# Performance work log

Hardware: AMD Instinct MI355X
Metric: run time of the kernel (lower is better)

## Reference

```python
import jax, jax.numpy as jnp
import numpy as np

N_NODES = 50000
N_EDGES = 800000
F_NODE = 128
F_TASK = 128
HID = 64
HEADS = 4
BATCH = 16
NEG_SLOPE = 0.2


def setup_inputs() -> dict:
    key = jax.random.key(0)
    ks = jax.random.split(key, 20)
    rn = lambda k, sh, s=0.05: jax.random.normal(k, sh, dtype=jnp.float32) * s
    return {
        "x": rn(ks[0], (N_NODES, F_NODE), 1.0),
        "edge_index": jax.random.randint(ks[1], (2, N_EDGES), 0, N_NODES, dtype=jnp.int32),
        "task_feat": rn(ks[2], (BATCH, F_TASK), 1.0),
        # GAT layer 1 (F_NODE -> HEADS*HID, concat)
        "W1": rn(ks[3], (F_NODE, HEADS * HID)),
        "att_src1": rn(ks[4], (HEADS, HID)),
        "att_dst1": rn(ks[5], (HEADS, HID)),
        "b1": jnp.zeros((HEADS * HID,), jnp.float32),
        # GAT layer 2 (HEADS*HID -> HID, 1 head, mean/no-concat)
        "W2": rn(ks[6], (HEADS * HID, HID)),
        "att_src2": rn(ks[7], (1, HID)),
        "att_dst2": rn(ks[8], (1, HID)),
        "b2": jnp.zeros((HID,), jnp.float32),
        # task encoder MLP
        "te_W1": rn(ks[9], (F_TASK, HID)),
        "te_b1": jnp.zeros((HID,), jnp.float32),
        "te_W2": rn(ks[10], (HID, HID)),
        "te_b2": jnp.zeros((HID,), jnp.float32),
        # classifier MLP (2*HID -> HID -> 1)
        "cl_W1": rn(ks[11], (2 * HID, HID)),
        "cl_b1": jnp.zeros((HID,), jnp.float32),
        "cl_W2": rn(ks[12], (HID, 1)),
        "cl_b2": jnp.zeros((1,), jnp.float32),
    }


def _gat(x, src, dst, W, a_src, a_dst, bias, concat):
    """PyG-style GATConv: self-loops, per-dst segment softmax, scatter-add."""
    n = x.shape[0]
    heads, ch = a_src.shape
    h = (x @ W).reshape(n, heads, ch)                       # [N,H,C]
    alpha_s = jnp.einsum("nhc,hc->nh", h, a_src)            # [N,H]
    alpha_d = jnp.einsum("nhc,hc->nh", h, a_dst)
    loop = jnp.arange(n, dtype=src.dtype)                   # add self-loops
    s = jnp.concatenate([src, loop])
    d = jnp.concatenate([dst, loop])
    e = jax.nn.leaky_relu(alpha_s[s] + alpha_d[d], NEG_SLOPE)   # [E+N,H]
    m = jax.lax.stop_gradient(jax.ops.segment_max(e, d, num_segments=n))
    ex = jnp.exp(e - m[d])
    den = jax.ops.segment_sum(ex, d, num_segments=n)
    alpha = ex / (den[d] + 1e-16)                           # [E+N,H]
    out = jax.ops.segment_sum(h[s] * alpha[:, :, None], d, num_segments=n)
    out = out.reshape(n, heads * ch) if concat else out.mean(axis=1)
    return out + bias


def reference(x, edge_index, task_feat, W1, att_src1, att_dst1, b1,
              W2, att_src2, att_dst2, b2, te_W1, te_b1, te_W2, te_b2,
              cl_W1, cl_b1, cl_W2, cl_b2):
    src, dst = edge_index[0], edge_index[1]
    h = jax.nn.elu(_gat(x, src, dst, W1, att_src1, att_dst1, b1, True))
    h = jax.nn.elu(_gat(h, src, dst, W2, att_src2, att_dst2, b2, False))  # [N,HID]
    t = jax.nn.relu(task_feat @ te_W1 + te_b1) @ te_W2 + te_b2            # [B,HID]
    # classifier on concat([h_exp, t_exp]) == split first linear into two halves
    Wh, Wt = cl_W1[:HID], cl_W1[HID:]
    z = jax.nn.relu((h @ Wh)[None, :, :] + (t @ Wt)[:, None, :] + cl_b1)  # [B,N,HID]
    scores = (z @ cl_W2)[..., 0] + cl_b2[0]                               # [B,N]
    return scores
```

## Files before the change

### kernel.cpp

```cpp
#include <hip/hip_runtime.h>
#include <hip/hip_fp16.h>

#define NN 50000
#define NE 800000
#define FN 128
#define HH 256
#define HID 64
#define NBKT 196
#define CHUNK 4000
#define REGCAP 8192

typedef _Float16 f16x8 __attribute__((ext_vector_type(8)));
typedef float f32x4 __attribute__((ext_vector_type(4)));

__device__ __forceinline__ float lrelu(float v){ return v >= 0.f ? v : 0.2f * v; }
__device__ __forceinline__ float elu_(float v){ return v > 0.f ? v : expm1f(v); }

__device__ __forceinline__ void unp4(const float2 r, float& f0, float& f1, float& f2, float& f3){
  const __half2* hp = (const __half2*)&r;
  float2 a = __half22float2(hp[0]);
  float2 b = __half22float2(hp[1]);
  f0 = a.x; f1 = a.y; f2 = b.x; f3 = b.y;
}

__global__ void k_misc(const float* __restrict__ W2, const float* __restrict__ W1,
                       __half* __restrict__ Bp, __half* __restrict__ Bp1, __half* __restrict__ Bwh,
                       const float* __restrict__ task, const float* __restrict__ W1t,
                       const float* __restrict__ b1t, const float* __restrict__ W2t,
                       const float* __restrict__ b2t, const float* __restrict__ clW1,
                       const float* __restrict__ clb1, float* __restrict__ tWb,
                       int* __restrict__ binCnt){
  int bid = blockIdx.x, t = threadIdx.x;
  if (bid < 26){
    int f = bid * 256 + t;
    if (f < 2048){
      int lane = f & 63;
      int ct = (f >> 6) & 3, kt = f >> 8;
      int kbase = kt * 32 + (lane >> 4) * 8;
      int col = ct * 16 + (lane & 15);
#pragma unroll
      for (int i = 0; i < 8; ++i)
        Bp[(size_t)f * 8 + i] = (__half)W2[(kbase + i) * HID + col];
    } else if (f < 6144){
      int g = f - 2048;
      int lane = g & 63;
      int ct = (g >> 6) & 15, kt = g >> 10;
      int kbase = kt * 32 + (lane >> 4) * 8;
      int col = ct * 16 + (lane & 15);
#pragma unroll
      for (int i = 0; i < 8; ++i)
        Bp1[(size_t)g * 8 + i] = (__half)W1[(kbase + i) * HH + col];
    } else {
      int g = f - 6144;
      int lane = g & 63;
      int ct = (g >> 6) & 3, kt = g >> 8;
      int kbase = kt * 32 + (lane >> 4) * 8;
      int col = ct * 16 + (lane & 15);
#pragma unroll
      for (int i = 0; i < 8; ++i)
        Bwh[(size_t)g * 8 + i] = (__half)clW1[(kbase + i) * HID + col];
    }
  } else {
    binCnt[t] = 0;
    __shared__ float t1[16][64];
    __shared__ float t2[16][64];
    for (int idx = t; idx < 1024; idx += 256){
      int b = idx >> 6, c = idx & 63;
      float acc = b1t[c];
      for (int k = 0; k < 128; ++k) acc = fmaf(task[b*128 + k], W1t[k*64 + c], acc);
      t1[b][c] = fmaxf(acc, 0.f);
    }
    __syncthreads();
    for (int idx = t; idx < 1024; idx += 256){
      int b = idx >> 6, c = idx & 63;
      float acc = b2t[c];
      for (int k = 0; k < 64; ++k) acc = fmaf(t1[b][k], W2t[k*64 + c], acc);
      t2[b][c] = acc;
    }
    __syncthreads();
    for (int idx = t; idx < 1024; idx += 256){
      int b = idx >> 6, c = idx & 63;
      float acc = clb1[c];
      for (int k = 0; k < 64; ++k) acc = fmaf(t2[b][k], clW1[(64 + k)*64 + c], acc);
      tWb[idx] = acc;
    }
  }
}

__global__ void k_binGemm(const int* __restrict__ ei, int* __restrict__ binCnt,
                          unsigned* __restrict__ pr,
                          const float* __restrict__ x, const __half* __restrict__ Bp1,
                          const float* __restrict__ as1, const float* __restrict__ ad1,
                          __half* __restrict__ h1h, float* __restrict__ als, float* __restrict__ ald){
  __shared__ int hist[NBKT];
  __shared__ int lstart[NBKT];
  __shared__ int gpos[NBKT];
  __shared__ int cnt[NBKT];
  __shared__ unsigned stage[CHUNK];
  int bid = blockIdx.x, t = threadIdx.x;
  if (bid < 200){
    int e_base = bid * CHUNK;
    if (t < NBKT){ hist[t] = 0; cnt[t] = 0; }
    __syncthreads();
    for (int i = t; i < CHUNK; i += 256)
      atomicAdd(&hist[ei[NE + e_base + i] >> 8], 1);
    __syncthreads();
    {
      int lane = t & 63, wvi = t >> 6;
      int v = (t < NBKT) ? hist[t] : 0;
      int iv = v;
#pragma unroll
      for (int off = 1; off < 64; off <<= 1){
        int u = __shfl_up(iv, off);
        if (lane >= off) iv += u;
      }
      __shared__ int wsum[4];
      if (lane == 63) wsum[wvi] = iv;
      __syncthreads();
      int add = 0;
      for (int w = 0; w < wvi; ++w) add += wsum[w];
      iv += add;
      if (t < NBKT){
        lstart[t] = iv - v;
        gpos[t] = (v > 0) ? atomicAdd(&binCnt[t], v) : 0;
      }
    }
    __syncthreads();
    for (int i = t; i < CHUNK; i += 256){
      int e = e_base + i;
      int s = ei[e], d = ei[NE + e];
      int bb = d >> 8;
      int r = atomicAdd(&cnt[bb], 1);
      stage[lstart[bb] + r] = (unsigned)s | ((unsigned)(d & 255) << 16) | ((unsigned)bb << 24);
    }
    __syncthreads();
    for (int i = t; i < CHUNK; i += 256){
      unsigned p = stage[i];
      int bb = p >> 24;
      pr[(size_t)bb * REGCAP + gpos[bb] + (i - lstart[bb])] = p;
    }
    return;
  }
  int blk = bid - 200;
  int wv = t >> 6, lane = t & 63;
  int n0 = blk * 64 + wv * 16;
  int arow = n0 + (lane & 15);
  if (arow > NN - 1) arow = NN - 1;
  const float* xbase = x + (size_t)arow * FN + (lane >> 4) * 8;
  const f16x8* bbase = (const f16x8*)Bp1 + lane;

  f32x4 acc[16];
#pragma unroll
  for (int ct = 0; ct < 16; ++ct) acc[ct] = (f32x4){0.f,0.f,0.f,0.f};

#pragma unroll
  for (int kt = 0; kt < 4; ++kt){
    float4 xa = *(const float4*)(xbase + kt * 32);
    float4 xb = *(const float4*)(xbase + kt * 32 + 4);
    f16x8 a;
    a[0] = (_Float16)xa.x; a[1] = (_Float16)xa.y; a[2] = (_Float16)xa.z; a[3] = (_Float16)xa.w;
    a[4] = (_Float16)xb.x; a[5] = (_Float16)xb.y; a[6] = (_Float16)xb.z; a[7] = (_Float16)xb.w;
#pragma unroll
    for (int ct = 0; ct < 16; ++ct)
      acc[ct] = __builtin_amdgcn_mfma_f32_16x16x32_f16(a, bbase[(kt*16 + ct) * 64], acc[ct], 0, 0, 0);
  }

  int c4 = lane & 15, g4 = lane >> 4;
#pragma unroll
  for (int ct = 0; ct < 16; ++ct){
#pragma unroll
    for (int i = 0; i < 4; ++i){
      int n = n0 + g4 * 4 + i;
      if (n < NN) h1h[(size_t)n * HH + ct * 16 + c4] = (__half)acc[ct][i];
    }
  }
#pragma unroll
  for (int h = 0; h < 4; ++h){
    float sa0 = as1[(h*4+0)*16 + c4], sa1 = as1[(h*4+1)*16 + c4];
    float sa2 = as1[(h*4+2)*16 + c4], sa3 = as1[(h*4+3)*16 + c4];
    float da0 = ad1[(h*4+0)*16 + c4], da1 = ad1[(h*4+1)*16 + c4];
    float da2 = ad1[(h*4+2)*16 + c4], da3 = ad1[(h*4+3)*16 + c4];
#pragma unroll
    for (int i = 0; i < 4; ++i){
      float vs = acc[h*4+0][i]*sa0 + acc[h*4+1][i]*sa1 + acc[h*4+2][i]*sa2 + acc[h*4+3][i]*sa3;
      float vd = acc[h*4+0][i]*da0 + acc[h*4+1][i]*da1 + acc[h*4+2][i]*da2 + acc[h*4+3][i]*da3;
#pragma unroll
      for (int off = 1; off < 16; off <<= 1){
        vs += __shfl_xor(vs, off);
        vd += __shfl_xor(vd, off);
      }
      if (c4 == 0){
        int n = n0 + g4 * 4 + i;
        if (n < NN){ als[n*4 + h] = vs; ald[n*4 + h] = vd; }
      }
    }
  }
}

__global__ void k_rsplace(const int* __restrict__ binCnt, const unsigned* __restrict__ pr,
                          int* __restrict__ rs, int* __restrict__ csr){
  __shared__ int bbase[256];
  __shared__ int hist[256];
  __shared__ int lp[256];
  __shared__ int wsA[4];
  __shared__ int wsB[4];
  int b = blockIdx.x, t = threadIdx.x;
  int lane = t & 63, wv = t >> 6;
  {
    int v = (t < NBKT) ? binCnt[t] : 0;
    int iv = v;
#pragma unroll
    for (int off = 1; off < 64; off <<= 1){
      int u = __shfl_up(iv, off);
      if (lane >= off) iv += u;
    }
    if (lane == 63) wsA[wv] = iv;
    __syncthreads();
    int add = 0;
    for (int w = 0; w < wv; ++w) add += wsA[w];
    bbase[t] = iv + add - v;
    hist[t] = 0;
  }
  __syncthreads();
  int myBase = bbase[b];
  int myCnt  = binCnt[b];
  const unsigned* reg = pr + (size_t)b * REGCAP;
  for (int i = t; i < myCnt; i += 256)
    atomicAdd(&hist[(reg[i] >> 16) & 255], 1);
  __syncthreads();
  int excl;
  {
    int v = hist[t];
    int iv = v;
#pragma unroll
    for (int off = 1; off < 64; off <<= 1){
      int u = __shfl_up(iv, off);
      if (lane >= off) iv += u;
    }
    if (lane == 63) wsB[wv] = iv;
    __syncthreads();
    int add = 0;
    for (int w = 0; w < wv; ++w) add += wsB[w];
    excl = myBase + iv + add - v;
    lp[t] = excl;
  }
  int idx = b * 256 + t;
  if (idx < NN) rs[idx] = excl;
  if (b == 0 && t == 0) rs[NN] = NE;
  __syncthreads();
  for (int i = t; i < myCnt; i += 256){
    unsigned p = reg[i];
    int pos = atomicAdd(&lp[(p >> 16) & 255], 1);
    csr[pos] = (int)(p & 0xFFFFu);
  }
}

__global__ void k_agg1m(const int* __restrict__ rs, const int* __restrict__ csr,
                        const __half* __restrict__ h1h, const float* __restrict__ als,
                        const float* __restrict__ ald, const float* __restrict__ b1,
                        __half* __restrict__ g1h){
  int t = threadIdx.x, wv = t >> 6, lane = t & 63;
  int head = lane >> 4, q = lane & 15;
  int n = blockIdx.x * 4 + wv;
  int e0 = rs[n], e1 = rs[n + 1];
  int deg = e1 - e0;
  float adh = ald[n*4 + head];

  float w0r = 0.f, w1r = 0.f, w2r = 0.f, w3r = 0.f;
  int   s0r = 0,   s1r = 0,   s2r = 0,   s3r = 0;
  float den = 0.f;
  if (q      < deg){ s0r = csr[e0 + q];      w0r = expf(lrelu(als[s0r*4+head] + adh)); den += w0r; }
  if (q + 16 < deg){ s1r = csr[e0 + 16 + q]; w1r = expf(lrelu(als[s1r*4+head] + adh)); den += w1r; }
  if (q + 32 < deg){ s2r = csr[e0 + 32 + q]; w2r = expf(lrelu(als[s2r*4+head] + adh)); den += w2r; }
  if (q + 48 < deg){ s3r = csr[e0 + 48 + q]; w3r = expf(lrelu(als[s3r*4+head] + adh)); den += w3r; }
  for (int e = e0 + 64 + q; e < e1; e += 16) den += expf(lrelu(als[csr[e]*4+head] + adh));
  den += __shfl_xor(den, 1); den += __shfl_xor(den, 2);
  den += __shfl_xor(den, 4); den += __shfl_xor(den, 8);
  float selfw = expf(lrelu(als[n*4+head] + adh));
  float inv = 1.f / (den + selfw + 1e-16f);
  float wself = selfw * inv;

  float a0, a1, a2, a3;
  { float2 r = *(const float2*)(h1h + (size_t)n * HH + lane * 4);
    float f0,f1,f2,f3; unp4(r, f0,f1,f2,f3);
    a0 = wself*f0; a1 = wself*f1; a2 = wself*f2; a3 = wself*f3; }

  int hb = lane & 48;
  int cnt = deg < 64 ? deg : 64;
  auto pass = [&](float wp, int sp, int off){
    int lim = cnt - off; if (lim <= 0) return; if (lim > 16) lim = 16;
    for (int q2 = 0; q2 < lim; q2 += 4){
      int j1 = q2 + 1, j2 = q2 + 2, j3 = q2 + 3;
      float m1 = (j1 < lim) ? inv : 0.f; if (j1 >= lim) j1 = q2;
      float m2 = (j2 < lim) ? inv : 0.f; if (j2 >= lim) j2 = q2;
      float m3 = (j3 < lim) ? inv : 0.f; if (j3 >= lim) j3 = q2;
      float wa = inv * __shfl(wp, hb + q2); int sa = __shfl(sp, hb + q2);
      float wb = m1  * __shfl(wp, hb + j1); int sb = __shfl(sp, hb + j1);
      float wc = m2  * __shfl(wp, hb + j2); int sc = __shfl(sp, hb + j2);
      float wd = m3  * __shfl(wp, hb + j3); int sd = __shfl(sp, hb + j3);
      float2 ra = *(const float2*)(h1h + (size_t)sa * HH + lane * 4);
      float2 rb = *(const float2*)(h1h + (size_t)sb * HH + lane * 4);
      float2 rc = *(const float2*)(h1h + (size_t)sc * HH + lane * 4);
      float2 rd = *(const float2*)(h1h + (size_t)sd * HH + lane * 4);
      float f0,f1,f2,f3;
      unp4(ra, f0,f1,f2,f3); a0=fmaf(wa,f0,a0); a1=fmaf(wa,f1,a1); a2=fmaf(wa,f2,a2); a3=fmaf(wa,f3,a3);
      unp4(rb, f0,f1,f2,f3); a0=fmaf(wb,f0,a0); a1=fmaf(wb,f1,a1); a2=fmaf(wb,f2,a2); a3=fmaf(wb,f3,a3);
      unp4(rc, f0,f1,f2,f3); a0=fmaf(wc,f0,a0); a1=fmaf(wc,f1,a1); a2=fmaf(wc,f2,a2); a3=fmaf(wc,f3,a3);
      unp4(rd, f0,f1,f2,f3); a0=fmaf(wd,f0,a0); a1=fmaf(wd,f1,a1); a2=fmaf(wd,f2,a2); a3=fmaf(wd,f3,a3);
    }
  };
  pass(w0r, s0r, 0); pass(w1r, s1r, 16); pass(w2r, s2r, 32); pass(w3r, s3r, 48);
  for (int e = e0 + 64; e < e1; ++e){
    int s = csr[e];
    float w = inv * expf(lrelu(als[s*4+head] + adh));
    float2 r = *(const float2*)(h1h + (size_t)s * HH + lane * 4);
    float f0,f1,f2,f3; unp4(r, f0,f1,f2,f3);
    a0=fmaf(w,f0,a0); a1=fmaf(w,f1,a1); a2=fmaf(w,f2,a2); a3=fmaf(w,f3,a3);
  }

  float4 b4 = *(const float4*)(b1 + lane * 4);
  __half2 p0 = __floats2half2_rn(elu_(a0 + b4.x), elu_(a1 + b4.y));
  __half2 p1 = __floats2half2_rn(elu_(a2 + b4.z), elu_(a3 + b4.w));
  float2 outv; ((__half2*)&outv)[0] = p0; ((__half2*)&outv)[1] = p1;
  *(float2*)(g1h + (size_t)n * HH + lane * 4) = outv;
}

__global__ void k_gemm2m(const __half* __restrict__ g1h, const __half* __restrict__ Bp,
                         const float* __restrict__ as2, const float* __restrict__ ad2,
                         __half* __restrict__ h2h, float* __restrict__ als2, float* __restrict__ ald2){
  int t = threadIdx.x, wv = t >> 6, lane = t & 63;
  int n0 = blockIdx.x * 64 + wv * 16;
  int arow = n0 + (lane & 15);
  if (arow > NN - 1) arow = NN - 1;
  const _Float16* gbase = (const _Float16*)g1h + (size_t)arow * HH + (lane >> 4) * 8;
  const f16x8* bbase = (const f16x8*)Bp + lane;

  f32x4 acc0 = {0.f,0.f,0.f,0.f}, acc1 = {0.f,0.f,0.f,0.f};
  f32x4 acc2 = {0.f,0.f,0.f,0.f}, acc3 = {0.f,0.f,0.f,0.f};
#pragma unroll
  for (int kt = 0; kt < 8; ++kt){
    f16x8 a = *(const f16x8*)(gbase + kt * 32);
    acc0 = __builtin_amdgcn_mfma_f32_16x16x32_f16(a, bbase[(kt*4 + 0) * 64], acc0, 0, 0, 0);
    acc1 = __builtin_amdgcn_mfma_f32_16x16x32_f16(a, bbase[(kt*4 + 1) * 64], acc1, 0, 0, 0);
    acc2 = __builtin_amdgcn_mfma_f32_16x16x32_f16(a, bbase[(kt*4 + 2) * 64], acc2, 0, 0, 0);
    acc3 = __builtin_amdgcn_mfma_f32_16x16x32_f16(a, bbase[(kt*4 + 3) * 64], acc3, 0, 0, 0);
  }
  int c4 = lane & 15, g4 = lane >> 4;
  float as2v0 = as2[c4], as2v1 = as2[16 + c4], as2v2 = as2[32 + c4], as2v3 = as2[48 + c4];
  float ad2v0 = ad2[c4], ad2v1 = ad2[16 + c4], ad2v2 = ad2[32 + c4], ad2v3 = ad2[48 + c4];
  float vs[4], vd[4];
#pragma unroll
  for (int i = 0; i < 4; ++i){
    int n = n0 + g4 * 4 + i;
    if (n < NN){
      h2h[(size_t)n * HID + c4]      = (__half)acc0[i];
      h2h[(size_t)n * HID + 16 + c4] = (__half)acc1[i];
      h2h[(size_t)n * HID + 32 + c4] = (__half)acc2[i];
      h2h[(size_t)n * HID + 48 + c4] = (__half)acc3[i];
    }
    vs[i] = acc0[i]*as2v0 + acc1[i]*as2v1 + acc2[i]*as2v2 + acc3[i]*as2v3;
    vd[i] = acc0[i]*ad2v0 + acc1[i]*ad2v1 + acc2[i]*ad2v2 + acc3[i]*ad2v3;
  }
#pragma unroll
  for (int off = 1; off < 16; off <<= 1){
#pragma unroll
    for (int i = 0; i < 4; ++i){
      vs[i] += __shfl_xor(vs[i], off);
      vd[i] += __shfl_xor(vd[i], off);
    }
  }
  if (c4 == 0){
#pragma unroll
    for (int i = 0; i < 4; ++i){
      int n = n0 + g4 * 4 + i;
      if (n < NN){ als2[n] = vs[i]; ald2[n] = vd[i]; }
    }
  }
}

#define OSTRIDE 72
__global__ void k_agg2f(const int* __restrict__ rs, const int* __restrict__ csr,
                        const __half* __restrict__ h2h, const float* __restrict__ als,
                        const float* __restrict__ ald, const float* __restrict__ b2,
                        const __half* __restrict__ Bwh, const float* __restrict__ tWb,
                        const float* __restrict__ w2, const float* __restrict__ b2s,
                        float* __restrict__ out){
  __shared__ __half o_lds[64 * OSTRIDE];
  __shared__ float tws[1024];
  __shared__ float w2s[64];
  int t = threadIdx.x, lane = t & 63, wv = t >> 6;
  for (int i = t; i < 1024; i += 256) tws[i] = tWb[i];
  if (t < 64) w2s[t] = w2[t];

  int q = lane & 15;
  int g = t >> 4;
  int n0b = blockIdx.x * 64;
  int gb = lane & 48;
#pragma unroll 1
  for (int j = 0; j < 4; ++j){
    int nl = g * 4 + j;
    int n = n0b + nl;
    int nc = (n < NN) ? n : NN - 1;
    int e0 = rs[nc], e1 = rs[nc + 1];
    int deg = e1 - e0;
    float adn = ald[nc];

    float w0r = 0.f, w1r = 0.f, w2r = 0.f, w3r = 0.f;
    int   s0r = 0,   s1r = 0,   s2r = 0,   s3r = 0;
    float den = 0.f;
    if (q      < deg){ s0r = csr[e0 + q];      w0r = expf(lrelu(als[s0r] + adn)); den += w0r; }
    if (q + 16 < deg){ s1r = csr[e0 + 16 + q]; w1r = expf(lrelu(als[s1r] + adn)); den += w1r; }
    if (q + 32 < deg){ s2r = csr[e0 + 32 + q]; w2r = expf(lrelu(als[s2r] + adn)); den += w2r; }
    if (q + 48 < deg){ s3r = csr[e0 + 48 + q]; w3r = expf(lrelu(als[s3r] + adn)); den += w3r; }
    for (int e = e0 + 64 + q; e < e1; e += 16) den += expf(lrelu(als[csr[e]] + adn));
    den += __shfl_xor(den, 1); den += __shfl_xor(den, 2);
    den += __shfl_xor(den, 4); den += __shfl_xor(den, 8);
    float selfw = expf(lrelu(als[nc] + adn));
    float inv = 1.f / (den + selfw + 1e-16f);
    float wself = selfw * inv;

    float a0, a1, a2, a3;
    { float2 r = *(const float2*)(h2h + (size_t)nc * HID + q * 4);
      float f0,f1,f2,f3; unp4(r, f0,f1,f2,f3);
      a0 = wself*f0; a1 = wself*f1; a2 = wself*f2; a3 = wself*f3; }

    int dmax = deg;
    dmax = max(dmax, __shfl_xor(dmax, 16));
    dmax = max(dmax, __shfl_xor(dmax, 32));
    int cnt = dmax < 64 ? dmax : 64;
    auto pass = [&](float wp, int sp, int off){
      int lim = cnt - off; if (lim <= 0) return; if (lim > 16) lim = 16;
      for (int jj = 0; jj < lim; jj += 4){
        int j1 = jj + 1, j2 = jj + 2, j3 = jj + 3;
        float m1 = (j1 < lim) ? inv : 0.f; if (j1 >= lim) j1 = jj;
        float m2 = (j2 < lim) ? inv : 0.f; if (j2 >= lim) j2 = jj;
        float m3 = (j3 < lim) ? inv : 0.f; if (j3 >= lim) j3 = jj;
        float wa = inv * __shfl(wp, gb + jj); int sa = __shfl(sp, gb + jj);
        float wb = m1  * __shfl(wp, gb + j1); int sb = __shfl(sp, gb + j1);
        float wc = m2  * __shfl(wp, gb + j2); int sc = __shfl(sp, gb + j2);
        float wd = m3  * __shfl(wp, gb + j3); int sd = __shfl(sp, gb + j3);
        float2 ra = *(const float2*)(h2h + (size_t)sa * HID + q * 4);
        float2 rb = *(const float2*)(h2h + (size_t)sb * HID + q * 4);
        float2 rc = *(const float2*)(h2h + (size_t)sc * HID + q * 4);
        float2 rd = *(const float2*)(h2h + (size_t)sd * HID + q * 4);
        float f0,f1,f2,f3;
        unp4(ra, f0,f1,f2,f3); a0=fmaf(wa,f0,a0); a1=fmaf(wa,f1,a1); a2=fmaf(wa,f2,a2); a3=fmaf(wa,f3,a3);
        unp4(rb, f0,f1,f2,f3); a0=fmaf(wb,f0,a0); a1=fmaf(wb,f1,a1); a2=fmaf(wb,f2,a2); a3=fmaf(wb,f3,a3);
        unp4(rc, f0,f1,f2,f3); a0=fmaf(wc,f0,a0); a1=fmaf(wc,f1,a1); a2=fmaf(wc,f2,a2); a3=fmaf(wc,f3,a3);
        unp4(rd, f0,f1,f2,f3); a0=fmaf(wd,f0,a0); a1=fmaf(wd,f1,a1); a2=fmaf(wd,f2,a2); a3=fmaf(wd,f3,a3);
      }
    };
    pass(w0r, s0r, 0); pass(w1r, s1r, 16); pass(w2r, s2r, 32); pass(w3r, s3r, 48);
    for (int e = e0 + 64; e < e1; ++e){
      int s = csr[e];
      float w = inv * expf(lrelu(als[s] + adn));
      float2 r = *(const float2*)(h2h + (size_t)s * HID + q * 4);
      float f0,f1,f2,f3; unp4(r, f0,f1,f2,f3);
      a0=fmaf(w,f0,a0); a1=fmaf(w,f1,a1); a2=fmaf(w,f2,a2); a3=fmaf(w,f3,a3);
    }

    float4 b4 = *(const float4*)(b2 + q * 4);
    __half2 p0 = __floats2half2_rn(elu_(a0 + b4.x), elu_(a1 + b4.y));
    __half2 p1 = __floats2half2_rn(elu_(a2 + b4.z), elu_(a3 + b4.w));
    float2 outv; ((__half2*)&outv)[0] = p0; ((__half2*)&outv)[1] = p1;
    *(float2*)(o_lds + nl * OSTRIDE + q * 4) = outv;
  }
  __syncthreads();

  const _Float16* obase = (const _Float16*)o_lds + (wv * 16 + (lane & 15)) * OSTRIDE + (lane >> 4) * 8;
  const f16x8* bbase = (const f16x8*)Bwh + lane;

  f32x4 acc[4];
#pragma unroll
  for (int ct = 0; ct < 4; ++ct) acc[ct] = (f32x4){0.f,0.f,0.f,0.f};
#pragma unroll
  for (int kt = 0; kt < 2; ++kt){
    f16x8 a = *(const f16x8*)(obase + kt * 32);
#pragma unroll
    for (int ct = 0; ct < 4; ++ct)
      acc[ct] = __builtin_amdgcn_mfma_f32_16x16x32_f16(a, bbase[(kt*4 + ct) * 64], acc[ct], 0, 0, 0);
  }
  int c4 = lane & 15, g4 = lane >> 4;
  float wv0 = w2s[c4], wv1 = w2s[16 + c4], wv2 = w2s[32 + c4], wv3 = w2s[48 + c4];
  float bias = b2s[0];
#pragma unroll
  for (int i = 0; i < 4; ++i){
    int n = n0b + wv * 16 + g4 * 4 + i;
    float v[16];
#pragma unroll
    for (int b = 0; b < 16; ++b){
      const float* twb = tws + b * 64;
      v[b] = fmaxf(acc[0][i] + twb[c4], 0.f)      * wv0
           + fmaxf(acc[1][i] + twb[16 + c4], 0.f) * wv1
           + fmaxf(acc[2][i] + twb[32 + c4], 0.f) * wv2
           + fmaxf(acc[3][i] + twb[48 + c4], 0.f) * wv3;
    }
    bool h3 = (lane & 8) != 0;
    float u[8];
#pragma unroll
    for (int jj = 0; jj < 8; ++jj){
      float keep = h3 ? v[jj+8] : v[jj];
      float send = h3 ? v[jj]   : v[jj+8];
      u[jj] = keep + __shfl_xor(send, 8);
    }
    bool h2b = (lane & 4) != 0;
    float p[4];
#pragma unroll
    for (int jj = 0; jj < 4; ++jj){
      float keep = h2b ? u[jj+4] : u[jj];
      float send = h2b ? u[jj]   : u[jj+4];
      p[jj] = keep + __shfl_xor(send, 4);
    }
    bool h1b = (lane & 2) != 0;
    float qq[2];
#pragma unroll
    for (int jj = 0; jj < 2; ++jj){
      float keep = h1b ? p[jj+2] : p[jj];
      float send = h1b ? p[jj]   : p[jj+2];
      qq[jj] = keep + __shfl_xor(send, 2);
    }
    bool h0 = (lane & 1) != 0;
    float keep = h0 ? qq[1] : qq[0];
    float send = h0 ? qq[0] : qq[1];
    float z = keep + __shfl_xor(send, 1);
    if (n < NN) out[(size_t)c4 * NN + n] = z + bias;
  }
}

extern "C" void kernel_launch(void* const* d_in, const int* in_sizes, int n_in,
                              void* d_out, int out_size, void* d_ws, size_t ws_size,
                              hipStream_t stream){
  const float* x    = (const float*)d_in[0];
  const int*   ei   = (const int*)  d_in[1];
  const float* task = (const float*)d_in[2];
  const float* W1   = (const float*)d_in[3];
  const float* as1  = (const float*)d_in[4];
  const float* ad1  = (const float*)d_in[5];
  const float* b1   = (const float*)d_in[6];
  const float* W2   = (const float*)d_in[7];
  const float* as2  = (const float*)d_in[8];
  const float* ad2  = (const float*)d_in[9];
  const float* b2   = (const float*)d_in[10];
  const float* teW1 = (const float*)d_in[11];
  const float* teb1 = (const float*)d_in[12];
  const float* teW2 = (const float*)d_in[13];
  const float* teb2 = (const float*)d_in[14];
  const float* clW1 = (const float*)d_in[15];
  const float* clb1 = (const float*)d_in[16];
  const float* clW2 = (const float*)d_in[17];
  const float* clb2 = (const float*)d_in[18];
  float* out = (float*)d_out;
  float* ws  = (float*)d_ws;

  __half* h1h  = (__half*)ws;
  float* als1  = ws + 6400000;
  float* ald1  = als1 + 200000;
  __half* g1h  = (__half*)(ald1 + 200000);
  __half* h2h  = (__half*)(ald1 + 200000 + 6400000);
  float* als2  = ald1 + 200000 + 6400000 + 1600000;
  float* ald2  = als2 + 50000;
  float* tWb   = ald2 + 50000;
  int*   rs    = (int*)(tWb + 1024);
  int*   csr   = rs + 50004;
  int*   binCnt= csr + 800000;
  __half* Bp   = (__half*)(binCnt + 256);
  __half* Bp1  = Bp + 16384;
  __half* Bwh  = Bp1 + 32768;
  unsigned* pr = (unsigned*)(Bwh + 4096);

  k_misc   <<<27, 256, 0, stream>>>(W2, W1, Bp, Bp1, Bwh,
                                    task, teW1, teb1, teW2, teb2, clW1, clb1, tWb, binCnt);
  k_binGemm<<<200 + (NN + 63)/64, 256, 0, stream>>>(ei, binCnt, pr, x, Bp1,
                                                    as1, ad1, h1h, als1, ald1);
  k_rsplace<<<NBKT, 256, 0, stream>>>(binCnt, pr, rs, csr);
  k_agg1m  <<<12500, 256, 0, stream>>>(rs, csr, h1h, als1, ald1, b1, g1h);
  k_gemm2m <<<(NN + 63)/64, 256, 0, stream>>>(g1h, Bp, as2, ad2, h2h, als2, ald2);
  k_agg2f  <<<(NN + 63)/64, 256, 0, stream>>>(rs, csr, h2h, als2, ald2, b2,
                                              Bwh, tWb, clW2, clb2, out);
}
```

Measured before the change: 170.6 us.

## Fuse layer-1 aggregation with layer-2 GEMM through LDS tile

Merges the layer-1 attention aggregation kernel and the layer-2 MFMA GEMM into one kernel. Each block aggregates 16 nodes (4 per wave, looped), writes the ELU'd fp16 features to shared memory, then each wave computes one 16-column slice of the 16x64 GEMM and the attention logits via an LDS reduction. This removes the g1h global round trip (write then read of N*256 halves) and one launch, at the cost of serialising four nodes per wave and adding two block barriers.

After: 164.7 us (median of 2 runs). 3.5% less time.

```diff
diff --git a/kernel.cpp b/kernel.cpp
--- a/kernel.cpp
+++ b/kernel.cpp
@@ -255,126 +255,122 @@
   }
 }
 
-__global__ void k_agg1m(const int* __restrict__ rs, const int* __restrict__ csr,
-                        const __half* __restrict__ h1h, const float* __restrict__ als,
-                        const float* __restrict__ ald, const float* __restrict__ b1,
-                        __half* __restrict__ g1h){
+#define GSTRIDE 264
+__global__ void k_agg1f2(const int* __restrict__ rs, const int* __restrict__ csr,
+                         const __half* __restrict__ h1h, const float* __restrict__ als,
+                         const float* __restrict__ ald, const float* __restrict__ b1,
+                         const __half* __restrict__ Bp, const float* __restrict__ as2,
+                         const float* __restrict__ ad2, __half* __restrict__ h2h,
+                         float* __restrict__ als2, float* __restrict__ ald2){
+  __shared__ __half g_lds[16 * GSTRIDE];
+  __shared__ float h2s[16][68];
   int t = threadIdx.x, wv = t >> 6, lane = t & 63;
   int head = lane >> 4, q = lane & 15;
-  int n = blockIdx.x * 4 + wv;
-  int e0 = rs[n], e1 = rs[n + 1];
-  int deg = e1 - e0;
-  float adh = ald[n*4 + head];
-
-  float w0r = 0.f, w1r = 0.f, w2r = 0.f, w3r = 0.f;
-  int   s0r = 0,   s1r = 0,   s2r = 0,   s3r = 0;
-  float den = 0.f;
-  if (q      < deg){ s0r = csr[e0 + q];      w0r = expf(lrelu(als[s0r*4+head] + adh)); den += w0r; }
-  if (q + 16 < deg){ s1r = csr[e0 + 16 + q]; w1r = expf(lrelu(als[s1r*4+head] + adh)); den += w1r; }
-  if (q + 32 < deg){ s2r = csr[e0 + 32 + q]; w2r = expf(lrelu(als[s2r*4+head] + adh)); den += w2r; }
-  if (q + 48 < deg){ s3r = csr[e0 + 48 + q]; w3r = expf(lrelu(als[s3r*4+head] + adh)); den += w3r; }
-  for (int e = e0 + 64 + q; e < e1; e += 16) den += expf(lrelu(als[csr[e]*4+head] + adh));
-  den += __shfl_xor(den, 1); den += __shfl_xor(den, 2);
-  den += __shfl_xor(den, 4); den += __shfl_xor(den, 8);
-  float selfw = expf(lrelu(als[n*4+head] + adh));
-  float inv = 1.f / (den + selfw + 1e-16f);
-  float wself = selfw * inv;
-
-  float a0, a1, a2, a3;
-  { float2 r = *(const float2*)(h1h + (size_t)n * HH + lane * 4);
-    float f0,f1,f2,f3; unp4(r, f0,f1,f2,f3);
-    a0 = wself*f0; a1 = wself*f1; a2 = wself*f2; a3 = wself*f3; }
-
   int hb = lane & 48;
-  int cnt = deg < 64 ? deg : 64;
-  auto pass = [&](float wp, int sp, int off){
-    int lim = cnt - off; if (lim <= 0) return; if (lim > 16) lim = 16;
-    for (int q2 = 0; q2 < lim; q2 += 4){
-      int j1 = q2 + 1, j2 = q2 + 2, j3 = q2 + 3;
-      float m1 = (j1 < lim) ? inv : 0.f; if (j1 >= lim) j1 = q2;
-      float m2 = (j2 < lim) ? inv : 0.f; if (j2 >= lim) j2 = q2;
-      float m3 = (j3 < lim) ? inv : 0.f; if (j3 >= lim) j3 = q2;
-      float wa = inv * __shfl(wp, hb + q2); int sa = __shfl(sp, hb + q2);
-      float wb = m1  * __shfl(wp, hb + j1); int sb = __shfl(sp, hb + j1);
-      float wc = m2  * __shfl(wp, hb + j2); int sc = __shfl(sp, hb + j2);
-      float wd = m3  * __shfl(wp, hb + j3); int sd = __shfl(sp, hb + j3);
-      float2 ra = *(const float2*)(h1h + (size_t)sa * HH + lane * 4);
-      float2 rb = *(const float2*)(h1h + (size_t)sb * HH + lane * 4);
-      float2 rc = *(const float2*)(h1h + (size_t)sc * HH + lane * 4);
-      float2 rd = *(const float2*)(h1h + (size_t)sd * HH + lane * 4);
-      float f0,f1,f2,f3;
-      unp4(ra, f0,f1,f2,f3); a0=fmaf(wa,f0,a0); a1=fmaf(wa,f1,a1); a2=fmaf(wa,f2,a2); a3=fmaf(wa,f3,a3);
-      unp4(rb, f0,f1,f2,f3); a0=fmaf(wb,f0,a0); a1=fmaf(wb,f1,a1); a2=fmaf(wb,f2,a2); a3=fmaf(wb,f3,a3);
-      unp4(rc, f0,f1,f2,f3); a0=fmaf(wc,f0,a0); a1=fmaf(wc,f1,a1); a2=fmaf(wc,f2,a2); a3=fmaf(wc,f3,a3);
-      unp4(rd, f0,f1,f2,f3); a0=fmaf(wd,f0,a0); a1=fmaf(wd,f1,a1); a2=fmaf(wd,f2,a2); a3=fmaf(wd,f3,a3);
-    }
-  };
-  pass(w0r, s0r, 0); pass(w1r, s1r, 16); pass(w2r, s2r, 32); pass(w3r, s3r, 48);
-  for (int e = e0 + 64; e < e1; ++e){
-    int s = csr[e];
-    float w = inv * expf(lrelu(als[s*4+head] + adh));
-    float2 r = *(const float2*)(h1h + (size_t)s * HH + lane * 4);
-    float f0,f1,f2,f3; unp4(r, f0,f1,f2,f3);
-    a0=fmaf(w,f0,a0); a1=fmaf(w,f1,a1); a2=fmaf(w,f2,a2); a3=fmaf(w,f3,a3);
-  }
-
-  float4 b4 = *(const float4*)(b1 + lane * 4);
-  __half2 p0 = __floats2half2_rn(elu_(a0 + b4.x), elu_(a1 + b4.y));
-  __half2 p1 = __floats2half2_rn(elu_(a2 + b4.z), elu_(a3 + b4.w));
-  float2 outv; ((__half2*)&outv)[0] = p0; ((__half2*)&outv)[1] = p1;
-  *(float2*)(g1h + (size_t)n * HH + lane * 4) = outv;
-}
-
-__global__ void k_gemm2m(const __half* __restrict__ g1h, const __half* __restrict__ Bp,
-                         const float* __restrict__ as2, const float* __restrict__ ad2,
-                         __half* __restrict__ h2h, float* __restrict__ als2, float* __restrict__ ald2){
-  int t = threadIdx.x, wv = t >> 6, lane = t & 63;
-  int n0 = blockIdx.x * 64 + wv * 16;
-  int arow = n0 + (lane & 15);
-  if (arow > NN - 1) arow = NN - 1;
-  const _Float16* gbase = (const _Float16*)g1h + (size_t)arow * HH + (lane >> 4) * 8;
+  int nblk = blockIdx.x * 16;
+
+#pragma unroll 1
+  for (int j = 0; j < 4; ++j){
+    int nl = wv * 4 + j;
+    int n = nblk + nl;
+    int e0 = rs[n], e1 = rs[n + 1];
+    int deg = e1 - e0;
+    float adh = ald[n*4 + head];
+
+    float w0r = 0.f, w1r = 0.f, w2r = 0.f, w3r = 0.f;
+    int   s0r = 0,   s1r = 0,   s2r = 0,   s3r = 0;
+    float den = 0.f;
+    if (q      < deg){ s0r = csr[e0 + q];      w0r = expf(lrelu(als[s0r*4+head] + adh)); den += w0r; }
+    if (q + 16 < deg){ s1r = csr[e0 + 16 + q]; w1r = expf(lrelu(als[s1r*4+head] + adh)); den += w1r; }
+    if (q + 32 < deg){ s2r = csr[e0 + 32 + q]; w2r = expf(lrelu(als[s2r*4+head] + adh)); den += w2r; }
+    if (q + 48 < deg){ s3r = csr[e0 + 48 + q]; w3r = expf(lrelu(als[s3r*4+head] + adh)); den += w3r; }
+    for (int e = e0 + 64 + q; e < e1; e += 16) den += expf(lrelu(als[csr[e]*4+head] + adh));
+    den += __shfl_xor(den, 1); den += __shfl_xor(den, 2);
+    den += __shfl_xor(den, 4); den += __shfl_xor(den, 8);
+    float selfw = expf(lrelu(als[n*4+head] + adh));
+    float inv = 1.f / (den + selfw + 1e-16f);
+    float wself = selfw * inv;
+
+    float a0, a1, a2, a3;
+    { float2 r = *(const float2*)(h1h + (size_t)n * HH + lane * 4);
+      float f0,f1,f2,f3; unp4(r, f0,f1,f2,f3);
+      a0 = wself*f0; a1 = wself*f1; a2 = wself*f2; a3 = wself*f3; }
+
+    int cnt = deg < 64 ? deg : 64;
+    auto pass = [&](float wp, int sp, int off){
+      int lim = cnt - off; if (lim <= 0) return; if (lim > 16) lim = 16;
+      for (int q2 = 0; q2 < lim; q2 += 4){
+        int j1 = q2 + 1, j2 = q2 + 2, j3 = q2 + 3;
+        float m1 = (j1 < lim) ? inv : 0.f; if (j1 >= lim) j1 = q2;
+        float m2 = (j2 < lim) ? inv : 0.f; if (j2 >= lim) j2 = q2;
+        float m3 = (j3 < lim) ? inv : 0.f; if (j3 >= lim) j3 = q2;
+        float wa = inv * __shfl(wp, hb + q2); int sa = __shfl(sp, hb + q2);
+        float wb = m1  * __shfl(wp, hb + j1); int sb = __shfl(sp, hb + j1);
+        float wc = m2  * __shfl(wp, hb + j2); int sc = __shfl(sp, hb + j2);
+        float wd = m3  * __shfl(wp, hb + j3); int sd = __shfl(sp, hb + j3);
+        float2 ra = *(const float2*)(h1h + (size_t)sa * HH + lane * 4);
+        float2 rb = *(const float2*)(h1h + (size_t)sb * HH + lane * 4);
+        float2 rc = *(const float2*)(h1h + (size_t)sc * HH + lane * 4);
+        float2 rd = *(const float2*)(h1h + (size_t)sd * HH + lane * 4);
+        float f0,f1,f2,f3;
+        unp4(ra, f0,f1,f2,f3); a0=fmaf(wa,f0,a0); a1=fmaf(wa,f1,a1); a2=fmaf(wa,f2,a2); a3=fmaf(wa,f3,a3);
+        unp4(rb, f0,f1,f2,f3); a0=fmaf(wb,f0,a0); a1=fmaf(wb,f1,a1); a2=fmaf(wb,f2,a2); a3=fmaf(wb,f3,a3);
+        unp4(rc, f0,f1,f2,f3); a0=fmaf(wc,f0,a0); a1=fmaf(wc,f1,a1); a2=fmaf(wc,f2,a2); a3=fmaf(wc,f3,a3);
+        unp4(rd, f0,f1,f2,f3); a0=fmaf(wd,f0,a0); a1=fmaf(wd,f1,a1); a2=fmaf(wd,f2,a2); a3=fmaf(wd,f3,a3);
+      }
+    };
+    pass(w0r, s0r, 0); pass(w1r, s1r, 16); pass(w2r, s2r, 32); pass(w3r, s3r, 48);
+    for (int e = e0 + 64; e < e1; ++e){
+      int s = csr[e];
+      float w = inv * expf(lrelu(als[s*4+head] + adh));
+      float2 r = *(const float2*)(h1h + (size_t)s * HH + lane * 4);
+      float f0,f1,f2,f3; unp4(r, f0,f1,f2,f3);
+      a0=fmaf(w,f0,a0); a1=fmaf(w,f1,a1); a2=fmaf(w,f2,a2); a3=fmaf(w,f3,a3);
+    }
+
+    float4 b4 = *(const float4*)(b1 + lane * 4);
+    __half2 p0 = __floats2half2_rn(elu_(a0 + b4.x), elu_(a1 + b4.y));
+    __half2 p1 = __floats2half2_rn(elu_(a2 + b4.z), elu_(a3 + b4.w));
+    float2 outv; ((__half2*)&outv)[0] = p0; ((__half2*)&outv)[1] = p1;
+    *(float2*)(g_lds + nl * GSTRIDE + lane * 4) = outv;
+  }
+  __syncthreads();
+
+  const _Float16* abase = (const _Float16*)g_lds + (lane & 15) * GSTRIDE + (lane >> 4) * 8;
   const f16x8* bbase = (const f16x8*)Bp + lane;
 
-  f32x4 acc0 = {0.f,0.f,0.f,0.f}, acc1 = {0.f,0.f,0.f,0.f};
-  f32x4 acc2 = {0.f,0.f,0.f,0.f}, acc3 = {0.f,0.f,0.f,0.f};
+  f32x4 acc = {0.f,0.f,0.f,0.f};
 #pragma unroll
   for (int kt = 0; kt < 8; ++kt){
-    f16x8 a = *(const f16x8*)(gbase + kt * 32);
-    acc0 = __builtin_amdgcn_mfma_f32_16x16x32_f16(a, bbase[(kt*4 + 0) * 64], acc0, 0, 0, 0);
-    acc1 = __builtin_amdgcn_mfma_f32_16x16x32_f16(a, bbase[(kt*4 + 1) * 64], acc1, 0, 0, 0);
-    acc2 = __builtin_amdgcn_mfma_f32_16x16x32_f16(a, bbase[(kt*4 + 2) * 64], acc2, 0, 0, 0);
-    acc3 = __builtin_amdgcn_mfma_f32_16x16x32_f16(a, bbase[(kt*4 + 3) * 64], acc3, 0, 0, 0);
+    f16x8 a = *(const f16x8*)(abase + kt * 32);
+    acc = __builtin_amdgcn_mfma_f32_16x16x32_f16(a, bbase[(kt*4 + wv) * 64], acc, 0, 0, 0);
   }
   int c4 = lane & 15, g4 = lane >> 4;
-  float as2v0 = as2[c4], as2v1 = as2[16 + c4], as2v2 = as2[32 + c4], as2v3 = as2[48 + c4];
-  float ad2v0 = ad2[c4], ad2v1 = ad2[16 + c4], ad2v2 = ad2[32 + c4], ad2v3 = ad2[48 + c4];
-  float vs[4], vd[4];
+  int col = wv * 16 + c4;
 #pragma unroll
   for (int i = 0; i < 4; ++i){
-    int n = n0 + g4 * 4 + i;
-    if (n < NN){
-      h2h[(size_t)n * HID + c4]      = (__half)acc0[i];
-      h2h[(size_t)n * HID + 16 + c4] = (__half)acc1[i];
-      h2h[(size_t)n * HID + 32 + c4] = (__half)acc2[i];
-      h2h[(size_t)n * HID + 48 + c4] = (__half)acc3[i];
-    }
-    vs[i] = acc0[i]*as2v0 + acc1[i]*as2v1 + acc2[i]*as2v2 + acc3[i]*as2v3;
-    vd[i] = acc0[i]*ad2v0 + acc1[i]*ad2v1 + acc2[i]*ad2v2 + acc3[i]*ad2v3;
-  }
-#pragma unroll
-  for (int off = 1; off < 16; off <<= 1){
-#pragma unroll
-    for (int i = 0; i < 4; ++i){
-      vs[i] += __shfl_xor(vs[i], off);
-      vd[i] += __shfl_xor(vd[i], off);
-    }
-  }
-  if (c4 == 0){
-#pragma unroll
-    for (int i = 0; i < 4; ++i){
-      int n = n0 + g4 * 4 + i;
-      if (n < NN){ als2[n] = vs[i]; ald2[n] = vd[i]; }
-    }
+    int nl = g4 * 4 + i;
+    h2h[(size_t)(nblk + nl) * HID + col] = (__half)acc[i];
+    h2s[nl][col] = acc[i];
+  }
+  __syncthreads();
+
+  int nl2 = t >> 4, l16 = t & 15;
+  float vs = 0.f, vd = 0.f;
+#pragma unroll
+  for (int k = 0; k < 4; ++k){
+    int c2 = l16 * 4 + k;
+    float hv = h2s[nl2][c2];
+    vs = fmaf(hv, as2[c2], vs);
+    vd = fmaf(hv, ad2[c2], vd);
+  }
+  vs += __shfl_xor(vs, 1); vd += __shfl_xor(vd, 1);
+  vs += __shfl_xor(vs, 2); vd += __shfl_xor(vd, 2);
+  vs += __shfl_xor(vs, 4); vd += __shfl_xor(vd, 4);
+  vs += __shfl_xor(vs, 8); vd += __shfl_xor(vd, 8);
+  if (l16 == 0){
+    int n = nblk + nl2;
+    als2[n] = vs; ald2[n] = vd;
   }
 }
 
@@ -555,9 +551,8 @@
   __half* h1h  = (__half*)ws;
   float* als1  = ws + 6400000;
   float* ald1  = als1 + 200000;
-  __half* g1h  = (__half*)(ald1 + 200000);
-  __half* h2h  = (__half*)(ald1 + 200000 + 6400000);
-  float* als2  = ald1 + 200000 + 6400000 + 1600000;
+  __half* h2h  = (__half*)(ald1 + 200000);
+  float* als2  = ald1 + 200000 + 1600000;
   float* ald2  = als2 + 50000;
   float* tWb   = ald2 + 50000;
   int*   rs    = (int*)(tWb + 1024);
@@ -573,8 +568,8 @@
   k_binGemm<<<200 + (NN + 63)/64, 256, 0, stream>>>(ei, binCnt, pr, x, Bp1,
                                                     as1, ad1, h1h, als1, ald1);
   k_rsplace<<<NBKT, 256, 0, stream>>>(binCnt, pr, rs, csr);
-  k_agg1m  <<<12500, 256, 0, stream>>>(rs, csr, h1h, als1, ald1, b1, g1h);
-  k_gemm2m <<<(NN + 63)/64, 256, 0, stream>>>(g1h, Bp, as2, ad2, h2h, als2, ald2);
+  k_agg1f2 <<<3125, 256, 0, stream>>>(rs, csr, h1h, als1, ald1, b1,
+                                      Bp, as2, ad2, h2h, als2, ald2);
   k_agg2f  <<<(NN + 63)/64, 256, 0, stream>>>(rs, csr, h2h, als2, ald2, b2,
                                               Bwh, tWb, clW2, clb2, out);
 }
```
